# Kernel optimization log

Measured on AMD Instinct MI355X. Metric: run time of the kernel, lower is better.

## Reference

```python
import jax, jax.numpy as jnp
import numpy as np
import math

S, B, D = 1024, 8, 512
H = 8
HD = D // H
DFF = 2048
NUM_BUCKETS = 32
MAX_DISTANCE = 128
LN_EPS = 1e-5


def setup_inputs() -> dict:
    key = jax.random.key(0)
    ks = jax.random.split(key, 12)
    s = 0.02
    return {
        "x": jax.random.normal(ks[0], (S, B, D), jnp.float32),
        "attn_mask": jnp.zeros((S, S), jnp.float32),
        "in_proj_w": jax.random.normal(ks[1], (3 * D, D), jnp.float32) * s,
        "in_proj_b": jnp.zeros((3 * D,), jnp.float32),
        "out_proj_w": jax.random.normal(ks[2], (D, D), jnp.float32) * s,
        "out_proj_b": jnp.zeros((D,), jnp.float32),
        "lin1_w": jax.random.normal(ks[3], (DFF, D), jnp.float32) * s,
        "lin1_b": jnp.zeros((DFF,), jnp.float32),
        "lin2_w": jax.random.normal(ks[4], (D, DFF), jnp.float32) * s,
        "lin2_b": jnp.zeros((D,), jnp.float32),
        "ln1_w": jnp.ones((D,), jnp.float32),
        "ln1_b": jnp.zeros((D,), jnp.float32),
        "ln2_w": jnp.ones((D,), jnp.float32),
        "ln2_b": jnp.zeros((D,), jnp.float32),
        "rel_emb": jax.random.normal(ks[5], (NUM_BUCKETS, H), jnp.float32) * s,
    }


def _relative_position_bucket(relative_position, num_buckets=NUM_BUCKETS, max_distance=MAX_DISTANCE):
    # bidirectional=True path (encoder)
    nb = num_buckets // 2
    rel_buckets = (relative_position > 0).astype(jnp.int32) * nb
    rp = jnp.abs(relative_position)
    max_exact = nb // 2
    is_small = rp < max_exact
    rp_safe = jnp.maximum(rp, 1)  # avoid log(0); masked by is_small below
    rp_large = max_exact + (
        jnp.log(rp_safe.astype(jnp.float32) / max_exact)
        / math.log(max_distance / max_exact)
        * (nb - max_exact)
    ).astype(jnp.int32)
    rp_large = jnp.minimum(rp_large, nb - 1)
    return rel_buckets + jnp.where(is_small, rp, rp_large)


def _compute_bias(rel_emb, q_len, k_len):
    ctx = jnp.arange(q_len, dtype=jnp.int32)[:, None]
    mem = jnp.arange(k_len, dtype=jnp.int32)[None, :]
    buckets = _relative_position_bucket(mem - ctx)          # [S, S]
    values = rel_emb[buckets]                                # [S, S, H]
    return jnp.transpose(values, (2, 0, 1))                  # [H, S, S]


def _layer_norm(x, w, b):
    mu = jnp.mean(x, axis=-1, keepdims=True)
    var = jnp.mean(jnp.square(x - mu), axis=-1, keepdims=True)
    return (x - mu) * jax.lax.rsqrt(var + LN_EPS) * w + b


def reference(x, attn_mask, in_proj_w, in_proj_b, out_proj_w, out_proj_b,
              lin1_w, lin1_b, lin2_w, lin2_b, ln1_w, ln1_b, ln2_w, ln2_b, rel_emb):
    s, b, d = x.shape
    # qkv projection (torch Linear: y = x W^T + b)
    qkv = x @ in_proj_w.T + in_proj_b                         # [S, B, 3D]
    q, k, v = jnp.split(qkv, 3, axis=-1)

    def to_bhsd(t):
        return jnp.transpose(t.reshape(s, b, H, HD), (1, 2, 0, 3))  # [B, H, S, HD]

    q, k, v = to_bhsd(q), to_bhsd(k), to_bhsd(v)
    scores = jnp.einsum("bhqd,bhkd->bhqk", q, k) / math.sqrt(HD)

    bias = _compute_bias(rel_emb, s, s)                       # [H, S, S]
    mask_bias = attn_mask[None, :, :] + bias                  # [H, S, S]
    attn = jax.nn.softmax(scores + mask_bias[None], axis=-1)  # [B, H, S, S]

    o = jnp.einsum("bhqk,bhkd->bhqd", attn, v)                # [B, H, S, HD]
    o = jnp.transpose(o, (2, 0, 1, 3)).reshape(s, b, d)       # [S, B, D]
    o = o @ out_proj_w.T + out_proj_b

    # post-norm (norm_first=False)
    y = _layer_norm(x + o, ln1_w, ln1_b)
    ff = jax.nn.relu(y @ lin1_w.T + lin1_b) @ lin2_w.T + lin2_b
    return _layer_norm(y + ff, ln2_w, ln2_b)
```

## Files before the change

kernel.cpp:

```cpp
#include <hip/hip_runtime.h>
#include <hip/hip_bf16.h>


#define S_LEN 1024
#define BATCH 8
#define DMODEL 512
#define NHEAD 8
#define HDIM 64
#define DFF 2048
#define NROWS (S_LEN * BATCH)

typedef __bf16 bf16x8 __attribute__((ext_vector_type(8)));
typedef short  s16x4  __attribute__((ext_vector_type(4)));
typedef float  f32x4  __attribute__((ext_vector_type(4)));

__device__ __forceinline__ void gload16(const void* g, void* l) {
    __builtin_amdgcn_global_load_lds(
        (const __attribute__((address_space(1))) void*)g,
        (__attribute__((address_space(3))) void*)l, 16, 0, 0);
}

__global__ __launch_bounds__(256)
void prep_embc_kernel(const float* __restrict__ x,
                      const float* __restrict__ wq, const float* __restrict__ wo,
                      const float* __restrict__ w1, const float* __restrict__ w2,
                      __hip_bfloat16* __restrict__ xb, __hip_bfloat16* __restrict__ wqb,
                      __hip_bfloat16* __restrict__ wob, __hip_bfloat16* __restrict__ w1b,
                      __hip_bfloat16* __restrict__ w2b,
                      const float* __restrict__ mask,
                      const float* __restrict__ rel_emb,
                      __hip_bfloat16* __restrict__ embC) {
    if (blockIdx.x < 7168) {
        const int NX = NROWS * DMODEL / 4;
        const int NQ = 3 * DMODEL * DMODEL / 4;
        const int NO = DMODEL * DMODEL / 4;
        const int N1 = DFF * DMODEL / 4;
        int i = blockIdx.x * 256 + threadIdx.x;
        const float* src; __hip_bfloat16* dst; int off;
        if (i < NX)                         { src = x;  dst = xb;  off = i; }
        else if ((i -= NX) < NQ)            { src = wq; dst = wqb; off = i; }
        else if ((i -= NQ) < NO)            { src = wo; dst = wob; off = i; }
        else if ((i -= NO) < N1)            { src = w1; dst = w1b; off = i; }
        else if ((i -= N1) < N1)            { src = w2; dst = w2b; off = i; }
        else return;
        float4 v = *(const float4*)(src + (size_t)off * 4);
        union { s16x4 s; __hip_bfloat16 b[4]; } u;
        u.b[0] = __float2bfloat16(v.x); u.b[1] = __float2bfloat16(v.y);
        u.b[2] = __float2bfloat16(v.z); u.b[3] = __float2bfloat16(v.w);
        *(s16x4*)(dst + (size_t)off * 4) = u.s;
    } else {
        int tid = (blockIdx.x - 7168) * 256 + threadIdx.x;
        int h  = tid >> 16;
        int r1 = tid & 65535;
        int qt = r1 >> 12;
        int w  = (r1 >> 10) & 3;
        int kb = (r1 >> 6) & 15;
        int lane = r1 & 63;
        int q = qt * 64 + w * 16 + (lane & 15);
        __hip_bfloat16 ov[16];
#pragma unroll
        for (int j = 0; j < 16; ++j) {
            int c = j >> 2, e = j & 3;
            int k = kb * 64 + c * 16 + (lane >> 4) * 4 + e;
            int rel = k - q;
            int bucket = (rel > 0) ? 16 : 0;
            int rp = rel < 0 ? -rel : rel;
            int v;
            if (rp < 8)          v = rp;
            else if (rp < 12)    v = 8;
            else if (rp < 16)    v = 9;
            else if (rp < 23)    v = 10;
            else if (rp < 32)    v = 11;
            else if (rp < 46)    v = 12;
            else if (rp < 64)    v = 13;
            else if (rp < 91)    v = 14;
            else                 v = 15;
            float bt = rel_emb[(bucket + v) * NHEAD + h];
            ov[j] = __float2bfloat16(__expf(mask[(size_t)q * S_LEN + k] + bt));
        }
        *(uint4*)(embC + (size_t)tid * 16) = *(uint4*)&ov[0];
        *(uint4*)(embC + (size_t)tid * 16 + 8) = *(uint4*)&ov[8];
    }
}

template <int MODE, bool RELU>
__global__ __launch_bounds__(512, 2)
void gemm256(const __hip_bfloat16* __restrict__ Ab,
             const __hip_bfloat16* __restrict__ Wb,
             const float* __restrict__ bias,
             void* __restrict__ outv,
             int M, int K) {
    const int id = blockIdx.x;
    const int by = id & 31;
    const int bx = id >> 5;
    const int w = threadIdx.x >> 6;
    const int lane = threadIdx.x & 63;
    const int m16 = lane & 15;
    const int quad = lane >> 4;
    const int wr = w >> 2;
    const int wc = w & 3;
    const int row0 = by * 256;
    const int col0 = bx * 256;

    __shared__ __align__(16) __bf16 As[2][256 * 64];
    __shared__ __align__(16) __bf16 Bs[2][256 * 64];

    const __bf16* Ap = (const __bf16*)Ab;
    const __bf16* Wp = (const __bf16*)Wb;

    const int r_in = lane >> 3;
    const int kb_sw = (lane & 7) ^ r_in;

    auto stageAh = [&](int k0, int hf, int p) {
#pragma unroll
        for (int i = 0; i < 2; ++i) {
            int grp = w * 2 + i;
            int row = hf * 128 + grp * 8 + r_in;
            gload16(Ap + (size_t)(row0 + row) * K + k0 + kb_sw * 8,
                    (void*)(&As[p][(hf * 128 + grp * 8) * 64]));
        }
    };
    auto stageBh = [&](int k0, int hf, int p) {
#pragma unroll
        for (int i = 0; i < 2; ++i) {
            int grp = w * 2 + i;
            int row = hf * 128 + grp * 8 + r_in;
            gload16(Wp + (size_t)(col0 + row) * K + k0 + kb_sw * 8,
                    (void*)(&Bs[p][(hf * 128 + grp * 8) * 64]));
        }
    };

    f32x4 acc[8][4];
#pragma unroll
    for (int mi = 0; mi < 8; ++mi)
#pragma unroll
        for (int ni = 0; ni < 4; ++ni) acc[mi][ni] = f32x4{0, 0, 0, 0};

    const int NT = K / 64;

    stageAh(0, 0, 0); stageAh(0, 1, 0);
    stageBh(0, 0, 0); stageBh(0, 1, 0);
    asm volatile("s_waitcnt vmcnt(0)" ::: "memory");
    __builtin_amdgcn_s_barrier();

    for (int t = 0; t < NT; ++t) {
        const int p = t & 1;
        const int kn = (t + 1) * 64;
        const bool pf = (t + 1 < NT);
#pragma unroll
        for (int q = 0; q < 4; ++q) {
            if (q == 0 && pf) { stageAh(kn, 0, p ^ 1); stageAh(kn, 1, p ^ 1); }
            if (q == 1 && pf) { stageBh(kn, 0, p ^ 1); stageBh(kn, 1, p ^ 1); }

            const int mh = q >> 1, nh = q & 1;
            bf16x8 af[2][4], bfr[2][2];
#pragma unroll
            for (int kk = 0; kk < 2; ++kk) {
                const int slot = (kk * 4 + quad) ^ (m16 & 7);
#pragma unroll
                for (int r = 0; r < 4; ++r) {
                    int row = wr * 128 + mh * 64 + r * 16 + m16;
                    af[kk][r] = *(const bf16x8*)(&As[p][row * 64 + slot * 8]);
                }
#pragma unroll
                for (int c = 0; c < 2; ++c) {
                    int col = wc * 64 + nh * 32 + c * 16 + m16;
                    bfr[kk][c] = *(const bf16x8*)(&Bs[p][col * 64 + slot * 8]);
                }
            }

            __builtin_amdgcn_s_barrier();

            __builtin_amdgcn_s_setprio(1);
#pragma unroll
            for (int kk = 0; kk < 2; ++kk)
#pragma unroll
                for (int c = 0; c < 2; ++c)
#pragma unroll
                    for (int r = 0; r < 4; ++r)
                        acc[mh * 4 + r][nh * 2 + c] =
                            __builtin_amdgcn_mfma_f32_16x16x32_bf16(
                                af[kk][r], bfr[kk][c], acc[mh * 4 + r][nh * 2 + c],
                                0, 0, 0);
            __builtin_amdgcn_s_setprio(0);
        }
        if (pf) asm volatile("s_waitcnt vmcnt(0)" ::: "memory");
        __builtin_amdgcn_s_barrier();
    }

#pragma unroll
    for (int ni = 0; ni < 4; ++ni) {
        int col = col0 + wc * 64 + ni * 16 + m16;
        float bv = bias[col];
#pragma unroll
        for (int mi = 0; mi < 8; ++mi) {
#pragma unroll
            for (int e = 0; e < 4; ++e) {
                int row = row0 + wr * 128 + mi * 16 + quad * 4 + e;
                float v = acc[mi][ni][e] + bv;
                if (RELU) v = fmaxf(v, 0.f);
                if (MODE == 1) {
                    ((__hip_bfloat16*)outv)[(size_t)row * M + col] = __float2bfloat16(v);
                } else {
                    int sect = col >> 9, h = (col >> 6) & 7, d = col & 63;
                    int s = row >> 3, bb = row & 7;
                    size_t idx;
                    if (sect == 2)
                        idx = (size_t)(128 + bb * 8 + h) * (S_LEN * HDIM)
                            + (size_t)d * S_LEN + s;
                    else
                        idx = ((size_t)(sect * 64 + bb * 8 + h) * S_LEN + s) * HDIM + d;
                    ((__hip_bfloat16*)outv)[idx] = __float2bfloat16(v);
                }
            }
        }
    }
}

template <int MODE, bool RELU>
__global__ __launch_bounds__(256)
void gemm_tile(const __hip_bfloat16* __restrict__ Ab,
               const __hip_bfloat16* __restrict__ Wb,
               const float* __restrict__ bias,
               void* __restrict__ outv,
               int N, int M, int Kloop, int Kstride) {
    const int id = blockIdx.x;
    int by, bx, bz;
    if (MODE == 0) { bz = id >> 8; int rem = id & 255; by = rem & 63; bx = rem >> 6; }
    else           { bz = 0; by = id & 63; bx = id >> 6; }
    const int w = threadIdx.x >> 6;
    const int lane = threadIdx.x & 63;
    const int m16 = lane & 15;
    const int quad = lane >> 4;
    const int row0 = by * 128;
    const int col0 = bx * 128;
    const int kbase = bz * Kloop;
    const int rowbase = (w >> 1) * 64;
    const int colbase = (w & 1) * 64;

    __shared__ __align__(16) __bf16 As[128 * 64];
    __shared__ __align__(16) __bf16 Bs[128 * 64];

    const __bf16* Ap = (const __bf16*)Ab;
    const __bf16* Wp = (const __bf16*)Wb;

    const int a_row_in_grp = lane >> 3;
    const int kb_sw = (lane & 7) ^ (lane >> 3);

    f32x4 acc[4][4];
#pragma unroll
    for (int c = 0; c < 4; ++c)
#pragma unroll
        for (int r = 0; r < 4; ++r) acc[c][r] = f32x4{0, 0, 0, 0};

    for (int k0 = 0; k0 < Kloop; k0 += 64) {
#pragma unroll
        for (int i = 0; i < 4; ++i) {
            int grp = w * 4 + i;
            int row = grp * 8 + a_row_in_grp;
            gload16(Ap + (size_t)(row0 + row) * Kstride + kbase + k0 + kb_sw * 8,
                    (void*)(As + grp * 512));
            gload16(Wp + (size_t)(col0 + row) * Kstride + kbase + k0 + kb_sw * 8,
                    (void*)(Bs + grp * 512));
        }
        __syncthreads();

#pragma unroll
        for (int kk = 0; kk < 2; ++kk) {
            bf16x8 af[4], bfr[4];
            int slot = (kk * 4 + quad) ^ (m16 & 7);
#pragma unroll
            for (int r = 0; r < 4; ++r)
                af[r] = *(const bf16x8*)(As + (rowbase + r * 16 + m16) * 64 + slot * 8);
#pragma unroll
            for (int c = 0; c < 4; ++c)
                bfr[c] = *(const bf16x8*)(Bs + (colbase + c * 16 + m16) * 64 + slot * 8);
#pragma unroll
            for (int c = 0; c < 4; ++c)
#pragma unroll
                for (int r = 0; r < 4; ++r)
                    acc[c][r] = __builtin_amdgcn_mfma_f32_16x16x32_bf16(
                        af[r], bfr[c], acc[c][r], 0, 0, 0);
        }
        __syncthreads();
    }

#pragma unroll
    for (int c = 0; c < 4; ++c) {
        int col = col0 + colbase + c * 16 + m16;
        float bv = (MODE == 0 && bz != 0) ? 0.f : bias[col];
#pragma unroll
        for (int r = 0; r < 4; ++r) {
#pragma unroll
            for (int e = 0; e < 4; ++e) {
                int row = row0 + rowbase + r * 16 + quad * 4 + e;
                float v = acc[c][r][e] + bv;
                if (RELU) v = fmaxf(v, 0.f);
                if (MODE == 0) {
                    ((float*)outv)[(size_t)bz * N * M + (size_t)row * M + col] = v;
                } else if (MODE == 1) {
                    ((__hip_bfloat16*)outv)[(size_t)row * M + col] = __float2bfloat16(v);
                } else {
                    int sect = col >> 9, h = (col >> 6) & 7, d = col & 63;
                    int s = row >> 3, bb = row & 7;
                    size_t idx;
                    if (sect == 2)
                        idx = (size_t)(128 + bb * 8 + h) * (S_LEN * HDIM)
                            + (size_t)d * S_LEN + s;
                    else
                        idx = ((size_t)(sect * 64 + bb * 8 + h) * S_LEN + s) * HDIM + d;
                    ((__hip_bfloat16*)outv)[idx] = __float2bfloat16(v);
                }
            }
        }
    }
}

__global__ __launch_bounds__(256)
void gemm64_db(const __hip_bfloat16* __restrict__ Ab,
               const __hip_bfloat16* __restrict__ Wb,
               const float* __restrict__ bias,
               float* __restrict__ outf,
               int N, int M, int K) {
    const int id = blockIdx.x;
    const int by = id & 63, bx = id >> 6;
    const int w = threadIdx.x >> 6;
    const int lane = threadIdx.x & 63;
    const int m16 = lane & 15;
    const int quad = lane >> 4;
    const int row0 = by * 128;
    const int col0 = bx * 64;
    const int rowbase = w * 32;

    __shared__ __align__(16) __bf16 As[2][128 * 64];
    __shared__ __align__(16) __bf16 Bs[2][64 * 64];

    const __bf16* Ap = (const __bf16*)Ab;
    const __bf16* Wp = (const __bf16*)Wb;

    const int a_row_in_grp = lane >> 3;
    const int kb_sw = (lane & 7) ^ (lane >> 3);

    auto stage = [&](int k0, int p) {
#pragma unroll
        for (int i = 0; i < 4; ++i) {
            int grp = w * 4 + i;
            int row = grp * 8 + a_row_in_grp;
            gload16(Ap + (size_t)(row0 + row) * K + k0 + kb_sw * 8,
                    (void*)(&As[p][grp * 512]));
        }
#pragma unroll
        for (int i = 0; i < 2; ++i) {
            int grp = w * 2 + i;
            int row = grp * 8 + a_row_in_grp;
            gload16(Wp + (size_t)(col0 + row) * K + k0 + kb_sw * 8,
                    (void*)(&Bs[p][grp * 512]));
        }
    };

    f32x4 acc[4][2];
#pragma unroll
    for (int c = 0; c < 4; ++c)
#pragma unroll
        for (int r = 0; r < 2; ++r) acc[c][r] = f32x4{0, 0, 0, 0};

    stage(0, 0);
    __syncthreads();

    int p = 0;
    for (int k0 = 0; k0 < K; k0 += 64, p ^= 1) {
        if (k0 + 64 < K) stage(k0 + 64, p ^ 1);
#pragma unroll
        for (int kk = 0; kk < 2; ++kk) {
            bf16x8 af[2], bfr[4];
            int slot = (kk * 4 + quad) ^ (m16 & 7);
#pragma unroll
            for (int r = 0; r < 2; ++r)
                af[r] = *(const bf16x8*)(&As[p][(rowbase + r * 16 + m16) * 64 + slot * 8]);
#pragma unroll
            for (int c = 0; c < 4; ++c)
                bfr[c] = *(const bf16x8*)(&Bs[p][(c * 16 + m16) * 64 + slot * 8]);
#pragma unroll
            for (int c = 0; c < 4; ++c)
#pragma unroll
                for (int r = 0; r < 2; ++r)
                    acc[c][r] = __builtin_amdgcn_mfma_f32_16x16x32_bf16(
                        af[r], bfr[c], acc[c][r], 0, 0, 0);
        }
        __syncthreads();
    }

#pragma unroll
    for (int c = 0; c < 4; ++c) {
        int col = col0 + c * 16 + m16;
        float bv = bias[col];
#pragma unroll
        for (int r = 0; r < 2; ++r)
#pragma unroll
            for (int e = 0; e < 4; ++e) {
                int row = row0 + rowbase + r * 16 + quad * 4 + e;
                outf[(size_t)row * M + col] = acc[c][r][e] + bv;
            }
    }
}

__global__ __launch_bounds__(256, 2)
void attn_mfma(const __hip_bfloat16* __restrict__ qkv_bhsd,
               const __hip_bfloat16* __restrict__ embC,
               __hip_bfloat16* __restrict__ o) {
    const int id = blockIdx.x;
    const int h = id & 7;
    const int qb = (id >> 3) & 7;
    const int b = id >> 6;
    const int bh = b * 8 + h;
    const int q0 = qb * 128;
    const int t = threadIdx.x;
    const int w = t >> 6, lane = t & 63, m16 = lane & 15, quad = lane >> 4;

    const __bf16* Qb  = (const __bf16*)qkv_bhsd + (size_t)bh * (S_LEN * HDIM);
    const __bf16* Kb  = (const __bf16*)qkv_bhsd + (size_t)(64 + bh) * (S_LEN * HDIM);
    const __bf16* VTg = (const __bf16*)qkv_bhsd + (size_t)(128 + bh) * (S_LEN * HDIM);
    const int qtA = qb * 2, qtB = qtA + 1;
    const __hip_bfloat16* ecA =
        embC + ((((size_t)h * 16 + qtA) * 4 + w) * 16) * 1024 + (size_t)lane * 16;
    const __hip_bfloat16* ecB =
        embC + ((((size_t)h * 16 + qtB) * 4 + w) * 16) * 1024 + (size_t)lane * 16;

    __shared__ __align__(16) __bf16 Ks[2][64 * 64];
    __shared__ __align__(16) __bf16 Vs[2][64 * 64];
    __shared__ __align__(16) __bf16 P[4][2][16 * 64];

    const int r_in = lane >> 3;
    const int kb_sw = (lane & 7) ^ r_in;

    auto stage = [&](int kc, int p) {
#pragma unroll
        for (int i = 0; i < 2; ++i) {
            int grp = w * 2 + i;
            gload16(Kb + (size_t)(kc + grp * 8 + r_in) * HDIM + kb_sw * 8,
                    (void*)(&Ks[p][grp * 512]));
            gload16(VTg + (size_t)(grp * 8 + r_in) * S_LEN + kc + kb_sw * 8,
                    (void*)(&Vs[p][grp * 512]));
        }
    };

    bf16x8 aQ0A, aQ1A, aQ0B, aQ1B;
    {
        const __bf16* qpA = Qb + (size_t)(q0 + w * 16 + m16) * HDIM + quad * 8;
        const __bf16* qpB = qpA + (size_t)64 * HDIM;
        bf16x8 t0 = *(const bf16x8*)qpA;
        bf16x8 t1 = *(const bf16x8*)(qpA + 32);
        bf16x8 t2 = *(const bf16x8*)qpB;
        bf16x8 t3 = *(const bf16x8*)(qpB + 32);
#pragma unroll
        for (int j = 0; j < 8; ++j) {
            t0[j] = (__bf16)((float)t0[j] * 0.125f);
            t1[j] = (__bf16)((float)t1[j] * 0.125f);
            t2[j] = (__bf16)((float)t2[j] * 0.125f);
            t3[j] = (__bf16)((float)t3[j] * 0.125f);
        }
        aQ0A = t0; aQ1A = t1; aQ0B = t2; aQ1B = t3;
    }

    f32x4 accOTA[4] = {f32x4{0,0,0,0}, f32x4{0,0,0,0}, f32x4{0,0,0,0}, f32x4{0,0,0,0}};
    f32x4 accOTB[4] = {f32x4{0,0,0,0}, f32x4{0,0,0,0}, f32x4{0,0,0,0}, f32x4{0,0,0,0}};
    float lpartA = 0.f, lpartB = 0.f;

    stage(0, 0);
    __syncthreads();

    int p = 0;
    for (int kc = 0; kc < S_LEN; kc += 64, p ^= 1) {
        if (kc + 64 < S_LEN) stage(kc + 64, p ^ 1);

        union { uint4 u[2]; __hip_bfloat16 e[16]; } evA, evB;
        evA.u[0] = *(const uint4*)(ecA + (size_t)(kc >> 6) * 1024);
        evA.u[1] = *(const uint4*)(ecA + (size_t)(kc >> 6) * 1024 + 8);
        evB.u[0] = *(const uint4*)(ecB + (size_t)(kc >> 6) * 1024);
        evB.u[1] = *(const uint4*)(ecB + (size_t)(kc >> 6) * 1024 + 8);

        f32x4 accTA[4] = {f32x4{0,0,0,0}, f32x4{0,0,0,0}, f32x4{0,0,0,0}, f32x4{0,0,0,0}};
        f32x4 accTB[4] = {f32x4{0,0,0,0}, f32x4{0,0,0,0}, f32x4{0,0,0,0}, f32x4{0,0,0,0}};
        const int sub = (m16 >> 3) * 512 + (m16 & 7) * 64;
        const int s0 = (quad ^ (m16 & 7)) * 8;
        const int s1 = ((4 + quad) ^ (m16 & 7)) * 8;
#pragma unroll
        for (int c = 0; c < 4; ++c) {
            const __bf16* kr = &Ks[p][c * 1024 + sub];
            bf16x8 b0 = *(const bf16x8*)(kr + s0);
            bf16x8 b1 = *(const bf16x8*)(kr + s1);
            accTA[c] = __builtin_amdgcn_mfma_f32_16x16x32_bf16(b0, aQ0A, accTA[c], 0, 0, 0);
            accTA[c] = __builtin_amdgcn_mfma_f32_16x16x32_bf16(b1, aQ1A, accTA[c], 0, 0, 0);
            accTB[c] = __builtin_amdgcn_mfma_f32_16x16x32_bf16(b0, aQ0B, accTB[c], 0, 0, 0);
            accTB[c] = __builtin_amdgcn_mfma_f32_16x16x32_bf16(b1, aQ1B, accTB[c], 0, 0, 0);
        }

#pragma unroll
        for (int c = 0; c < 4; ++c) {
            union { s16x4 s; __hip_bfloat16 bb[4]; } uA, uB;
#pragma unroll
            for (int e = 0; e < 4; ++e) {
                float pvA = __expf(accTA[c][e]) * __bfloat162float(evA.e[c * 4 + e]);
                float pvB = __expf(accTB[c][e]) * __bfloat162float(evB.e[c * 4 + e]);
                lpartA += pvA; lpartB += pvB;
                uA.bb[e] = __float2bfloat16(pvA);
                uB.bb[e] = __float2bfloat16(pvB);
            }
            int blk = (c * 2 + (quad >> 1)) ^ (m16 & 7);
            *(s16x4*)&P[w][0][m16 * 64 + blk * 8 + (quad & 1) * 4] = uA.s;
            *(s16x4*)&P[w][1][m16 * 64 + blk * 8 + (quad & 1) * 4] = uB.s;
        }

        bf16x8 pb0A = *(const bf16x8*)&P[w][0][m16 * 64 + ((quad) ^ (m16 & 7)) * 8];
        bf16x8 pb1A = *(const bf16x8*)&P[w][0][m16 * 64 + ((4 + quad) ^ (m16 & 7)) * 8];
        bf16x8 pb0B = *(const bf16x8*)&P[w][1][m16 * 64 + ((quad) ^ (m16 & 7)) * 8];
        bf16x8 pb1B = *(const bf16x8*)&P[w][1][m16 * 64 + ((4 + quad) ^ (m16 & 7)) * 8];

#pragma unroll
        for (int dt = 0; dt < 4; ++dt) {
            const __bf16* vr = &Vs[p][dt * 1024 + sub];
            bf16x8 v0 = *(const bf16x8*)(vr + s0);
            bf16x8 v1 = *(const bf16x8*)(vr + s1);
            accOTA[dt] = __builtin_amdgcn_mfma_f32_16x16x32_bf16(v0, pb0A, accOTA[dt], 0, 0, 0);
            accOTA[dt] = __builtin_amdgcn_mfma_f32_16x16x32_bf16(v1, pb1A, accOTA[dt], 0, 0, 0);
            accOTB[dt] = __builtin_amdgcn_mfma_f32_16x16x32_bf16(v0, pb0B, accOTB[dt], 0, 0, 0);
            accOTB[dt] = __builtin_amdgcn_mfma_f32_16x16x32_bf16(v1, pb1B, accOTB[dt], 0, 0, 0);
        }

        __syncthreads();
    }

    float lA = lpartA, lB = lpartB;
    lA += __shfl_xor(lA, 16); lA += __shfl_xor(lA, 32);
    lB += __shfl_xor(lB, 16); lB += __shfl_xor(lB, 32);
    float invA = 1.f / lA, invB = 1.f / lB;

    {
        int qA = q0 + w * 16 + m16;
        __hip_bfloat16* opA = o + ((size_t)qA * BATCH + b) * DMODEL + h * HDIM;
        __hip_bfloat16* opB = opA + (size_t)64 * BATCH * DMODEL;
#pragma unroll
        for (int dt = 0; dt < 4; ++dt) {
            union { s16x4 s; __hip_bfloat16 bb[4]; } uA, uB;
#pragma unroll
            for (int e = 0; e < 4; ++e) {
                uA.bb[e] = __float2bfloat16(accOTA[dt][e] * invA);
                uB.bb[e] = __float2bfloat16(accOTB[dt][e] * invB);
            }
            *(s16x4*)(opA + dt * 16 + quad * 4) = uA.s;
            *(s16x4*)(opB + dt * 16 + quad * 4) = uB.s;
        }
    }
}

__global__ __launch_bounds__(64)
void ln_kernel(const float* __restrict__ resid,
               const float* __restrict__ gin,
               const float* __restrict__ gin2,
               const float* __restrict__ w,
               const float* __restrict__ b,
               float* __restrict__ outf,
               __hip_bfloat16* __restrict__ outb) {
    const int row = blockIdx.x;
    const int lane = threadIdx.x;
    const float* rp = resid + (size_t)row * DMODEL;
    const float* gp = gin + (size_t)row * DMODEL;

    float4 v[2];
    float s = 0.f, s2 = 0.f;
#pragma unroll
    for (int i = 0; i < 2; ++i) {
        int d = i * 256 + lane * 4;
        float4 a = *(const float4*)(rp + d);
        float4 g = *(const float4*)(gp + d);
        a.x += g.x; a.y += g.y; a.z += g.z; a.w += g.w;
        if (gin2) {
            float4 g2 = *(const float4*)(gin2 + (size_t)row * DMODEL + d);
            a.x += g2.x; a.y += g2.y; a.z += g2.z; a.w += g2.w;
        }
        v[i] = a;
        s += a.x + a.y + a.z + a.w;
        s2 += a.x * a.x + a.y * a.y + a.z * a.z + a.w * a.w;
    }
#pragma unroll
    for (int off = 32; off; off >>= 1) {
        s  += __shfl_xor(s, off);
        s2 += __shfl_xor(s2, off);
    }
    float mu = s * (1.f / DMODEL);
    float var = s2 * (1.f / DMODEL) - mu * mu;
    float rs = rsqrtf(var + 1e-5f);
#pragma unroll
    for (int i = 0; i < 2; ++i) {
        int d = i * 256 + lane * 4;
        float4 wv = *(const float4*)(w + d);
        float4 bv = *(const float4*)(b + d);
        float4 y;
        y.x = (v[i].x - mu) * rs * wv.x + bv.x;
        y.y = (v[i].y - mu) * rs * wv.y + bv.y;
        y.z = (v[i].z - mu) * rs * wv.z + bv.z;
        y.w = (v[i].w - mu) * rs * wv.w + bv.w;
        *(float4*)(outf + (size_t)row * DMODEL + d) = y;
        if (outb) {
            union { s16x4 s4; __hip_bfloat16 e[4]; } u;
            u.e[0] = __float2bfloat16(y.x); u.e[1] = __float2bfloat16(y.y);
            u.e[2] = __float2bfloat16(y.z); u.e[3] = __float2bfloat16(y.w);
            *(s16x4*)(outb + (size_t)row * DMODEL + d) = u.s4;
        }
    }
}

extern "C" void kernel_launch(void* const* d_in, const int* in_sizes, int n_in,
                              void* d_out, int out_size, void* d_ws, size_t ws_size,
                              hipStream_t stream) {
    const float* x          = (const float*)d_in[0];
    const float* attn_mask  = (const float*)d_in[1];
    const float* in_proj_w  = (const float*)d_in[2];
    const float* in_proj_b  = (const float*)d_in[3];
    const float* out_proj_w = (const float*)d_in[4];
    const float* out_proj_b = (const float*)d_in[5];
    const float* lin1_w     = (const float*)d_in[6];
    const float* lin1_b     = (const float*)d_in[7];
    const float* lin2_w     = (const float*)d_in[8];
    const float* lin2_b     = (const float*)d_in[9];
    const float* ln1_w      = (const float*)d_in[10];
    const float* ln1_b      = (const float*)d_in[11];
    const float* ln2_w      = (const float*)d_in[12];
    const float* ln2_b      = (const float*)d_in[13];
    const float* rel_emb    = (const float*)d_in[14];

    char* ws = (char*)d_ws;
    size_t off = 0;
    auto alloc = [&](size_t bytes) {
        char* p = ws + off;
        off += (bytes + 255) / 256 * 256;
        return (void*)p;
    };
    __hip_bfloat16* embt  = (__hip_bfloat16*)alloc((size_t)NHEAD * S_LEN * S_LEN * 2);
    __hip_bfloat16* wqkvb = (__hip_bfloat16*)alloc((size_t)3 * DMODEL * DMODEL * 2);
    __hip_bfloat16* wob   = (__hip_bfloat16*)alloc((size_t)DMODEL * DMODEL * 2);
    __hip_bfloat16* w1b   = (__hip_bfloat16*)alloc((size_t)DFF * DMODEL * 2);
    __hip_bfloat16* w2b   = (__hip_bfloat16*)alloc((size_t)DMODEL * DFF * 2);
    __hip_bfloat16* xb    = (__hip_bfloat16*)alloc((size_t)NROWS * DMODEL * 2);
    __hip_bfloat16* qkvb  = (__hip_bfloat16*)alloc((size_t)3 * 64 * S_LEN * HDIM * 2);
    __hip_bfloat16* o     = (__hip_bfloat16*)alloc((size_t)NROWS * DMODEL * 2);
    float* tmp            = (float*)alloc((size_t)2 * NROWS * DMODEL * 4);
    float* yf             = (float*)alloc((size_t)NROWS * DMODEL * 4);
    __hip_bfloat16* yb    = (__hip_bfloat16*)alloc((size_t)NROWS * DMODEL * 2);
    __hip_bfloat16* ffb   = (__hip_bfloat16*)alloc((size_t)NROWS * DFF * 2);

    float* out = (float*)d_out;
    float* tmp2 = tmp + (size_t)NROWS * DMODEL;

    prep_embc_kernel<<<dim3(9216), 256, 0, stream>>>(
        x, in_proj_w, out_proj_w, lin1_w, lin2_w, xb, wqkvb, wob, w1b, w2b,
        attn_mask, rel_emb, embt);

    gemm256<2, false><<<dim3(192), 512, 0, stream>>>(
        xb, wqkvb, in_proj_b, qkvb, 3 * DMODEL, DMODEL);

    attn_mfma<<<dim3(512), 256, 0, stream>>>(qkvb, embt, o);

    gemm64_db<<<dim3(512), 256, 0, stream>>>(
        o, wob, out_proj_b, tmp, NROWS, DMODEL, DMODEL);

    ln_kernel<<<dim3(NROWS), 64, 0, stream>>>(x, tmp, nullptr, ln1_w, ln1_b, yf, yb);

    gemm256<1, true><<<dim3(256), 512, 0, stream>>>(
        yb, w1b, lin1_b, ffb, DFF, DMODEL);

    gemm_tile<0, false><<<dim3(512), 256, 0, stream>>>(
        ffb, w2b, lin2_b, tmp, NROWS, DMODEL, DFF / 2, DFF);

    ln_kernel<<<dim3(NROWS), 64, 0, stream>>>(yf, tmp, tmp2, ln2_w, ln2_b, out, nullptr);
}
```

Before: 295.8 us.

## Split GEMM tile loads per quadrant with partial vmcnt waits and fragment reuse

After: 296.7 us. No clear change (+0.3%).

```diff
diff --git a/kernel.cpp b/kernel.cpp
--- a/kernel.cpp
+++ b/kernel.cpp
@@ -83,6 +83,40 @@
     }
 }
 
+#define G256_READ_AF(MH)                                                        \
+    _Pragma("unroll")                                                           \
+    for (int kk = 0; kk < 2; ++kk) {                                            \
+        const int slot = (kk * 4 + quad) ^ (m16 & 7);                           \
+        _Pragma("unroll")                                                       \
+        for (int r = 0; r < 4; ++r)                                             \
+            af[kk][r] = *(const bf16x8*)(                                       \
+                &Asp[(wr * 128 + (MH) * 64 + r * 16 + m16) * 64 + slot * 8]);   \
+    }
+
+#define G256_READ_BF(NH, DST)                                                   \
+    _Pragma("unroll")                                                           \
+    for (int kk = 0; kk < 2; ++kk) {                                            \
+        const int slot = (kk * 4 + quad) ^ (m16 & 7);                           \
+        _Pragma("unroll")                                                       \
+        for (int c = 0; c < 2; ++c)                                             \
+            DST[kk][c] = *(const bf16x8*)(                                      \
+                &Bsp[(wc * 64 + (NH) * 32 + c * 16 + m16) * 64 + slot * 8]);    \
+    }
+
+#define G256_MFMA(MH, NH, BF)                                                   \
+    __builtin_amdgcn_s_setprio(1);                                              \
+    _Pragma("unroll")                                                           \
+    for (int kk = 0; kk < 2; ++kk)                                              \
+        _Pragma("unroll")                                                       \
+        for (int c = 0; c < 2; ++c)                                             \
+            _Pragma("unroll")                                                   \
+            for (int r = 0; r < 4; ++r)                                         \
+                acc[(MH) * 4 + r][(NH) * 2 + c] =                               \
+                    __builtin_amdgcn_mfma_f32_16x16x32_bf16(                    \
+                        af[kk][r], BF[kk][c], acc[(MH) * 4 + r][(NH) * 2 + c],  \
+                        0, 0, 0);                                               \
+    __builtin_amdgcn_s_setprio(0);
+
 template <int MODE, bool RELU>
 __global__ __launch_bounds__(512, 2)
 void gemm256(const __hip_bfloat16* __restrict__ Ab,
@@ -111,22 +145,21 @@
     const int r_in = lane >> 3;
     const int kb_sw = (lane & 7) ^ r_in;
 
-    auto stageAh = [&](int k0, int hf, int p) {
+    auto stageA2 = [&](int k0, int mh, int p) {
 #pragma unroll
         for (int i = 0; i < 2; ++i) {
-            int grp = w * 2 + i;
-            int row = hf * 128 + grp * 8 + r_in;
-            gload16(Ap + (size_t)(row0 + row) * K + k0 + kb_sw * 8,
-                    (void*)(&As[p][(hf * 128 + grp * 8) * 64]));
+            int rowb = i * 128 + mh * 64 + w * 8;
+            gload16(Ap + (size_t)(row0 + rowb + r_in) * K + k0 + kb_sw * 8,
+                    (void*)(&As[p][rowb * 64]));
         }
     };
-    auto stageBh = [&](int k0, int hf, int p) {
+    auto stageB2 = [&](int k0, int nh, int p) {
 #pragma unroll
         for (int i = 0; i < 2; ++i) {
-            int grp = w * 2 + i;
-            int row = hf * 128 + grp * 8 + r_in;
-            gload16(Wp + (size_t)(col0 + row) * K + k0 + kb_sw * 8,
-                    (void*)(&Bs[p][(hf * 128 + grp * 8) * 64]));
+            int g = w * 2 + i;
+            int rowb = (g >> 2) * 64 + nh * 32 + (g & 3) * 8;
+            gload16(Wp + (size_t)(col0 + rowb + r_in) * K + k0 + kb_sw * 8,
+                    (void*)(&Bs[p][rowb * 64]));
         }
     };
 
@@ -138,54 +171,43 @@
 
     const int NT = K / 64;
 
-    stageAh(0, 0, 0); stageAh(0, 1, 0);
-    stageBh(0, 0, 0); stageBh(0, 1, 0);
-    asm volatile("s_waitcnt vmcnt(0)" ::: "memory");
-    __builtin_amdgcn_s_barrier();
+    stageA2(0, 0, 0); stageB2(0, 0, 0); stageB2(0, 1, 0); stageA2(0, 1, 0);
 
     for (int t = 0; t < NT; ++t) {
         const int p = t & 1;
         const int kn = (t + 1) * 64;
         const bool pf = (t + 1 < NT);
-#pragma unroll
-        for (int q = 0; q < 4; ++q) {
-            if (q == 0 && pf) { stageAh(kn, 0, p ^ 1); stageAh(kn, 1, p ^ 1); }
-            if (q == 1 && pf) { stageBh(kn, 0, p ^ 1); stageBh(kn, 1, p ^ 1); }
-
-            const int mh = q >> 1, nh = q & 1;
-            bf16x8 af[2][4], bfr[2][2];
-#pragma unroll
-            for (int kk = 0; kk < 2; ++kk) {
-                const int slot = (kk * 4 + quad) ^ (m16 & 7);
-#pragma unroll
-                for (int r = 0; r < 4; ++r) {
-                    int row = wr * 128 + mh * 64 + r * 16 + m16;
-                    af[kk][r] = *(const bf16x8*)(&As[p][row * 64 + slot * 8]);
-                }
-#pragma unroll
-                for (int c = 0; c < 2; ++c) {
-                    int col = wc * 64 + nh * 32 + c * 16 + m16;
-                    bfr[kk][c] = *(const bf16x8*)(&Bs[p][col * 64 + slot * 8]);
-                }
-            }
-
-            __builtin_amdgcn_s_barrier();
-
-            __builtin_amdgcn_s_setprio(1);
-#pragma unroll
-            for (int kk = 0; kk < 2; ++kk)
-#pragma unroll
-                for (int c = 0; c < 2; ++c)
-#pragma unroll
-                    for (int r = 0; r < 4; ++r)
-                        acc[mh * 4 + r][nh * 2 + c] =
-                            __builtin_amdgcn_mfma_f32_16x16x32_bf16(
-                                af[kk][r], bfr[kk][c], acc[mh * 4 + r][nh * 2 + c],
-                                0, 0, 0);
-            __builtin_amdgcn_s_setprio(0);
-        }
-        if (pf) asm volatile("s_waitcnt vmcnt(0)" ::: "memory");
+        const __bf16* Asp = As[p];
+        const __bf16* Bsp = Bs[p];
+        bf16x8 af[2][4], bf0[2][2], bf1[2][2];
+
+        asm volatile("s_waitcnt vmcnt(4)" ::: "memory");
         __builtin_amdgcn_s_barrier();
+        __builtin_amdgcn_sched_barrier(0);
+        if (pf) stageA2(kn, 0, p ^ 1);
+        G256_READ_AF(0)
+        G256_READ_BF(0, bf0)
+        G256_MFMA(0, 0, bf0)
+
+        if (pf) { asm volatile("s_waitcnt vmcnt(4)" ::: "memory"); }
+        else    { asm volatile("s_waitcnt vmcnt(2)" ::: "memory"); }
+        __builtin_amdgcn_s_barrier();
+        __builtin_amdgcn_sched_barrier(0);
+        if (pf) stageB2(kn, 0, p ^ 1);
+        G256_READ_BF(1, bf1)
+        G256_MFMA(0, 1, bf1)
+
+        if (pf) { asm volatile("s_waitcnt vmcnt(4)" ::: "memory"); }
+        else    { asm volatile("s_waitcnt vmcnt(0)" ::: "memory"); }
+        __builtin_amdgcn_s_barrier();
+        __builtin_amdgcn_sched_barrier(0);
+        if (pf) stageB2(kn, 1, p ^ 1);
+        G256_READ_AF(1)
+        G256_MFMA(1, 0, bf0)
+
+        __builtin_amdgcn_s_barrier();
+        if (pf) stageA2(kn, 1, p ^ 1);
+        G256_MFMA(1, 1, bf1)
     }
 
 #pragma unroll
```
